# Performance work log

Hardware: AMD Instinct MI355X
Metric: run time of the kernel (lower is better)

Reference implementation:

```python
import jax, jax.numpy as jnp
import numpy as np

B, NS, S, H = 2048, 8, 8, 512   # batch, num_units, num_mem_slots, hidden==num_mem_size
WH, WK = 1, 32                  # write attention heads, key_size
RH, RK = 4, 32                  # read (mem) attention heads, mem_attention_key


def _lin(x, W, b):
    # torch nn.Linear convention: W is [out, in]
    return jnp.einsum('...i,oi->...o', x, W) + b


def setup_inputs() -> dict:
    key = jax.random.key(0)
    ks = jax.random.split(key, 13)
    def w(k, o, i):
        return jax.random.normal(k, (o, i), jnp.float32) * 0.02
    d = {
        'h_s': jax.random.normal(ks[0], (B, NS, H), jnp.float32),
        'mem': jax.random.normal(ks[1], (B, S, H), jnp.float32),
        'wq_w': w(ks[2], WH * WK, H), 'wq_b': jnp.zeros((WH * WK,), jnp.float32),
        'wk_w': w(ks[3], WH * WK, H), 'wk_b': jnp.zeros((WH * WK,), jnp.float32),
        'wv_w': w(ks[4], WH * H, H), 'wv_b': jnp.zeros((WH * H,), jnp.float32),
        'wo_w': w(ks[5], H, WH * H), 'wo_b': jnp.zeros((H,), jnp.float32),
        'ut_w': w(ks[6], H, H),      'ut_b': jnp.zeros((H,), jnp.float32),
        'ug_w': w(ks[7], 2 * H, H),  'ug_b': jnp.zeros((2 * H,), jnp.float32),
        'rq_w': w(ks[8], RH * RK, H), 'rq_b': jnp.zeros((RH * RK,), jnp.float32),
        'rk_w': w(ks[9], RH * RK, H), 'rk_b': jnp.zeros((RH * RK,), jnp.float32),
        'rv_w': w(ks[10], RH * H, H), 'rv_b': jnp.zeros((RH * H,), jnp.float32),
        'ro_w': w(ks[11], H, RH * H), 'ro_b': jnp.zeros((H,), jnp.float32),
    }
    return d


def _forward(h_s, mem, wq_w, wq_b, wk_w, wk_b, wv_w, wv_b, wo_w, wo_b,
             ut_w, ut_b, ug_w, ug_b, rq_w, rq_b, rk_w, rk_b, rv_w, rv_b,
             ro_w, ro_b):
    b = h_s.shape[0]
    T = NS + S  # concat length for write keys/values

    # ---------------- write ----------------
    xi = jnp.concatenate([h_s, mem], axis=1)                       # [B, T, H]
    q = _lin(mem, wq_w, wq_b).reshape(b, S, WH, WK).transpose(0, 2, 1, 3)   # [B,WH,S,WK]
    k = _lin(xi, wk_w, wk_b).reshape(b, T, WH, WK).transpose(0, 2, 1, 3)    # [B,WH,T,WK]
    v = _lin(xi, wv_w, wv_b).reshape(b, T, WH, H).transpose(0, 2, 1, 3)     # [B,WH,T,H]
    scores = jnp.einsum('bhsk,bhtk->bhst', q, k) / np.sqrt(WK).astype(np.float32)
    probs = jax.nn.softmax(scores, axis=-1)                         # [B,WH,S,T]
    ctx = jnp.einsum('bhst,bhtd->bhsd', probs, v)                   # [B,WH,S,H]
    ctx = ctx.transpose(0, 2, 1, 3).reshape(b, S, WH * H)
    mem_write = _lin(ctx, wo_w, wo_b)                               # [B,S,H]

    # ---------------- update (GRU-like gating) ----------------
    inputs_mean = jax.nn.relu(_lin(h_s, ut_w, ut_b)).mean(axis=1, keepdims=True)  # [B,1,H]
    kk = inputs_mean + jnp.tanh(mem)                                # [B,S,H]
    gates = jax.nn.sigmoid(_lin(kk, ug_w, ug_b))                    # [B,S,2H]
    input_gate, forget_gate = gates[..., :H], gates[..., H:]
    mem_new = input_gate * jnp.tanh(mem_write) + forget_gate * mem  # [B,S,H]

    # ---------------- read ----------------
    q = _lin(h_s, rq_w, rq_b).reshape(b, NS, RH, RK).transpose(0, 2, 1, 3)      # [B,RH,NS,RK]
    k = _lin(mem_new, rk_w, rk_b).reshape(b, S, RH, RK).transpose(0, 2, 1, 3)   # [B,RH,S,RK]
    v = _lin(mem_new, rv_w, rv_b).reshape(b, S, RH, H).transpose(0, 2, 1, 3)    # [B,RH,S,H]
    scores = jnp.einsum('bhnk,bhsk->bhns', q, k) / np.sqrt(RK).astype(np.float32)
    probs = jax.nn.softmax(scores, axis=-1)                          # [B,RH,NS,S]
    ctx = jnp.einsum('bhns,bhsd->bhnd', probs, v)                    # [B,RH,NS,H]
    ctx = ctx.transpose(0, 2, 1, 3).reshape(b, NS, RH * H)
    h_out = h_s + _lin(ctx, ro_w, ro_b)                              # residual
    return h_out, mem_new


def reference(h_s, mem, wq_w, wq_b, wk_w, wk_b, wv_w, wv_b, wo_w, wo_b,
              ut_w, ut_b, ug_w, ug_b, rq_w, rq_b, rk_w, rk_b, rv_w, rv_b,
              ro_w, ro_b):
    return _forward(h_s, mem, wq_w, wq_b, wk_w, wk_b, wv_w, wv_b, wo_w, wo_b,
                    ut_w, ut_b, ug_w, ug_b, rq_w, rq_b, rk_w, rk_b, rv_w, rv_b,
                    ro_w, ro_b)
```

## Files before the change

### kernel.cpp

```cpp
#include <hip/hip_runtime.h>

#define Bb   2048
#define Mrows 16384
#define Hd   512

typedef float  f32x4  __attribute__((ext_vector_type(4)));
typedef __bf16 bf16x8 __attribute__((ext_vector_type(8)));
typedef unsigned short us8 __attribute__((ext_vector_type(8)));

__device__ __forceinline__ unsigned short f2bf(float f) {
    unsigned int u = __builtin_bit_cast(unsigned int, f);
    u = u + 0x7FFFu + ((u >> 16) & 1u);
    return (unsigned short)(u >> 16);
}
__device__ __forceinline__ float bf2f(unsigned short h) {
    unsigned int u = ((unsigned int)h) << 16;
    return __builtin_bit_cast(float, u);
}

__device__ __forceinline__ void gload_lds16(const unsigned short* g, void* lds) {
    __builtin_amdgcn_global_load_lds(
        (const __attribute__((address_space(1))) unsigned int*)g,
        (__attribute__((address_space(3))) unsigned int*)lds,
        16, 0, 0);
}

#define MB (1024ull*1024ull)
#define OFF_WQ   0ull
#define OFF_WK   32768ull
#define OFF_WV   65536ull
#define OFF_WO   589824ull
#define OFF_UT   1114112ull
#define OFF_UG   1638400ull
#define OFF_RQ   2686976ull
#define OFF_RK   2818048ull
#define OFF_RV   2949120ull
#define OFF_RO   5046272ull
#define OFF_HS    (8*MB)
#define OFF_MEM   (24*MB)
#define OFF_UTR   (40*MB)
#define OFF_Q1    (60*MB)
#define OFF_K1    (62*MB)
#define OFF_V1    (66*MB)
#define OFF_CTX1  (100*MB)
#define OFF_KK    (116*MB)
#define OFF_TMW   (132*MB)
#define OFF_GATES (148*MB)
#define OFF_MNB   (180*MB)
#define OFF_Q2    (196*MB)
#define OFF_K2    (204*MB)
#define OFF_RVO   (40*MB)
#define OFF_CTX2  (104*MB)

struct CastSeg { const float* src; unsigned short* dst; int n4; };
struct CastParams { CastSeg seg[12]; };

__global__ __launch_bounds__(256) void cast_all(CastParams p) {
    CastSeg s = p.seg[blockIdx.y];
    int stride = gridDim.x * blockDim.x;
    for (int i = blockIdx.x * blockDim.x + threadIdx.x; i < s.n4; i += stride) {
        float4 v = reinterpret_cast<const float4*>(s.src)[i];
        ushort4 o;
        o.x = f2bf(v.x); o.y = f2bf(v.y); o.z = f2bf(v.z); o.w = f2bf(v.w);
        reinterpret_cast<ushort4*>(s.dst)[i] = o;
    }
}

template<int MODE>
__device__ __forceinline__ void store_c(void* out, const float* extra, int row,
                                        int col, int ldo, int remap_off, float v) {
    if (MODE == 0) {
        ((float*)out)[(size_t)row * ldo + col] = v;
    } else if (MODE == 1) {
        ((unsigned short*)out)[(size_t)row * ldo + col] = f2bf(v);
    } else if (MODE == 2) {
        ((unsigned short*)out)[(size_t)row * ldo + col] = f2bf(fmaxf(v, 0.f));
    } else if (MODE == 3) {
        ((unsigned short*)out)[(size_t)row * ldo + col] = f2bf(1.f / (1.f + expf(-v)));
    } else if (MODE == 4) {
        ((unsigned short*)out)[(size_t)row * ldo + col] = f2bf(tanhf(v));
    } else if (MODE == 5) {
        int rr = ((row >> 3) << 4) + (row & 7) + remap_off;
        ((float*)out)[(size_t)rr * ldo + col] = v;
    } else if (MODE == 6) {
        int rr = ((row >> 3) << 4) + (row & 7) + remap_off;
        ((unsigned short*)out)[(size_t)rr * ldo + col] = f2bf(v);
    } else if (MODE == 7) {
        ((float*)out)[(size_t)row * ldo + col] = v + extra[(size_t)row * ldo + col];
    }
}

struct GemmSeg {
    const unsigned short* A;
    const unsigned short* W;
    const float* bias;
    void* out;
    const float* extra;
    int mode, ldo, remap_off, tile0;
};
struct GemmParams { GemmSeg seg[4]; int nseg; int tiles_tot; };

template<int K>
__global__ __launch_bounds__(256, 4) void gemm_multi(GemmParams p)
{
    constexpr int NT = K / 32;
    __shared__ __align__(16) unsigned short As[2][128 * 32];
    __shared__ __align__(16) unsigned short Bs[2][128 * 32];

    const int nwg = (int)gridDim.x;
    const int swz = ((int)blockIdx.x & 7) * (nwg >> 3) + ((int)blockIdx.x >> 3);
    const int bm = swz / p.tiles_tot;
    const int tl = swz - bm * p.tiles_tot;

    int si = 0;
    #pragma unroll
    for (int i = 1; i < 4; i++)
        if (i < p.nseg && tl >= p.seg[i].tile0) si = i;
    const unsigned short* Aseg = p.seg[si].A;
    const unsigned short* Wseg = p.seg[si].W;
    const int bn = tl - p.seg[si].tile0;

    const int t = threadIdx.x;
    const int wave = t >> 6, lane = t & 63;
    const int wr = (wave >> 1) * 64;
    const int wc = (wave & 1) * 64;
    const int lrow = lane & 15;
    const int lkh  = lane >> 4;

    const unsigned short* ga[2];
    const unsigned short* gb[2];
    #pragma unroll
    for (int j = 0; j < 2; j++) {
        int c   = wave * 128 + j * 64 + lane;
        int row = c >> 2;
        int kl  = (c & 3) ^ (row & 3);
        ga[j] = Aseg + (size_t)(bm * 128 + row) * K + kl * 8;
        gb[j] = Wseg + (size_t)(bn * 128 + row) * K + kl * 8;
    }

    int aof[4], bof[4];
    #pragma unroll
    for (int m = 0; m < 4; m++) {
        int ra = wr + m * 16 + lrow;
        int rb = wc + m * 16 + lrow;
        aof[m] = ra * 32 + ((lkh ^ (ra & 3)) << 3);
        bof[m] = rb * 32 + ((lkh ^ (rb & 3)) << 3);
    }

    f32x4 acc[4][4] = {};

    #pragma unroll
    for (int j = 0; j < 2; j++) {
        gload_lds16(ga[j], (char*)As[0] + (wave * 2 + j) * 1024);
        gload_lds16(gb[j], (char*)Bs[0] + (wave * 2 + j) * 1024);
    }

    #pragma unroll 2
    for (int kt = 0; kt < NT; ++kt) {
        const int cur = kt & 1;
        asm volatile("s_waitcnt vmcnt(0)" ::: "memory");
        __builtin_amdgcn_s_barrier();
        __builtin_amdgcn_sched_barrier(0);
        if (kt + 1 < NT) {
            #pragma unroll
            for (int j = 0; j < 2; j++) {
                gload_lds16(ga[j] + (kt + 1) * 32, (char*)As[cur ^ 1] + (wave * 2 + j) * 1024);
                gload_lds16(gb[j] + (kt + 1) * 32, (char*)Bs[cur ^ 1] + (wave * 2 + j) * 1024);
            }
        }
        bf16x8 af[4], bfr[4];
        #pragma unroll
        for (int m = 0; m < 4; m++)
            af[m] = __builtin_bit_cast(bf16x8,
                        *reinterpret_cast<const us8*>(&As[cur][aof[m]]));
        #pragma unroll
        for (int n = 0; n < 4; n++)
            bfr[n] = __builtin_bit_cast(bf16x8,
                        *reinterpret_cast<const us8*>(&Bs[cur][bof[n]]));
        #pragma unroll
        for (int m = 0; m < 4; m++)
            #pragma unroll
            for (int n = 0; n < 4; n++)
                acc[m][n] = __builtin_amdgcn_mfma_f32_16x16x32_bf16(
                                af[m], bfr[n], acc[m][n], 0, 0, 0);
    }

    void* outp = p.seg[si].out;
    const float* bias = p.seg[si].bias;
    const float* extra = p.seg[si].extra;
    const int ldo = p.seg[si].ldo, rmo = p.seg[si].remap_off, mode = p.seg[si].mode;

    #define EPI(MODE_)                                                          \
        _Pragma("unroll")                                                       \
        for (int n = 0; n < 4; n++) {                                           \
            int col = bn * 128 + wc + n * 16 + lrow;                            \
            float bv = bias[col];                                               \
            _Pragma("unroll")                                                   \
            for (int m = 0; m < 4; m++) {                                       \
                _Pragma("unroll")                                               \
                for (int r = 0; r < 4; r++) {                                   \
                    int row = bm * 128 + wr + m * 16 + lkh * 4 + r;             \
                    store_c<MODE_>(outp, extra, row, col, ldo, rmo,             \
                                   acc[m][n][r] + bv);                          \
                }                                                               \
            }                                                                   \
        }
    switch (mode) {
        case 0: EPI(0) break;
        case 1: EPI(1) break;
        case 2: EPI(2) break;
        case 3: EPI(3) break;
        case 4: EPI(4) break;
        case 5: EPI(5) break;
        case 6: EPI(6) break;
        default: EPI(7) break;
    }
    #undef EPI
}

struct SmallSeg {
    const unsigned short* A;
    const unsigned short* W;
    const float* bias;
    float* out;
    int mode, remap_off;
};
struct SmallParams { SmallSeg seg[3]; };

__global__ __launch_bounds__(256) void gemm_small3(SmallParams p)
{
    constexpr int K = 512;
    const int si = blockIdx.x >> 8;
    const int bm = blockIdx.x & 255;
    const SmallSeg s = p.seg[si];

    const int wave = threadIdx.x >> 6;
    const int lane = threadIdx.x & 63;
    const int row0 = bm * 64 + wave * 16;
    const int lrow = lane & 15;
    const int lk   = (lane >> 4) << 3;

    f32x4 acc[2] = {};
    const unsigned short* ap  = s.A + (size_t)(row0 + lrow) * K + lk;
    const unsigned short* wp0 = s.W + (size_t)lrow * K + lk;

    #pragma unroll 4
    for (int ks = 0; ks < K; ks += 32) {
        bf16x8 af = __builtin_bit_cast(bf16x8,
                        *reinterpret_cast<const us8*>(ap + ks));
        #pragma unroll
        for (int tt = 0; tt < 2; tt++) {
            bf16x8 bfm = __builtin_bit_cast(bf16x8,
                        *reinterpret_cast<const us8*>(wp0 + (size_t)tt * 16 * K + ks));
            acc[tt] = __builtin_amdgcn_mfma_f32_16x16x32_bf16(af, bfm, acc[tt], 0, 0, 0);
        }
    }

    #pragma unroll
    for (int tt = 0; tt < 2; tt++) {
        int col = tt * 16 + lrow;
        float bv = s.bias[col];
        #pragma unroll
        for (int r = 0; r < 4; r++) {
            int row = row0 + (lane >> 4) * 4 + r;
            float v = acc[tt][r] + bv;
            if (s.mode == 0) {
                s.out[(size_t)row * 32 + col] = v;
            } else {
                int rr = ((row >> 3) << 4) + (row & 7) + s.remap_off;
                s.out[(size_t)rr * 32 + col] = v;
            }
        }
    }
}

__global__ __launch_bounds__(256) void meankk_kernel(
    const unsigned short* __restrict__ UTR, const float* __restrict__ mem,
    unsigned short* __restrict__ KK)
{
    int b = blockIdx.x;
    #pragma unroll
    for (int half = 0; half < 2; half++) {
        int j = threadIdx.x + half * 256;
        float sum = 0.f;
        #pragma unroll
        for (int r = 0; r < 8; r++)
            sum += bf2f(UTR[((size_t)(b * 8 + r) << 9) + j]);
        float mn = sum * 0.125f;
        #pragma unroll
        for (int r = 0; r < 8; r++) {
            size_t idx = ((size_t)(b * 8 + r) << 9) + j;
            KK[idx] = f2bf(mn + tanhf(mem[idx]));
        }
    }
}

__global__ __launch_bounds__(256) void memnew_kernel(
    const unsigned short* __restrict__ GATES, const unsigned short* __restrict__ TMW,
    const float* __restrict__ mem, float* __restrict__ out_mem,
    unsigned short* __restrict__ MNB)
{
    int idx = blockIdx.x * 256 + threadIdx.x;
    int m = idx >> 7, j4 = idx & 127;
    ushort4 ig4 = reinterpret_cast<const ushort4*>(GATES + (size_t)m * 1024)[j4];
    ushort4 fg4 = reinterpret_cast<const ushort4*>(GATES + (size_t)m * 1024 + 512)[j4];
    ushort4 tm4 = reinterpret_cast<const ushort4*>(TMW + (size_t)m * 512)[j4];
    float4  mm  = reinterpret_cast<const float4*>(mem + (size_t)m * 512)[j4];
    float4 v;
    v.x = bf2f(ig4.x) * bf2f(tm4.x) + bf2f(fg4.x) * mm.x;
    v.y = bf2f(ig4.y) * bf2f(tm4.y) + bf2f(fg4.y) * mm.y;
    v.z = bf2f(ig4.z) * bf2f(tm4.z) + bf2f(fg4.z) * mm.z;
    v.w = bf2f(ig4.w) * bf2f(tm4.w) + bf2f(fg4.w) * mm.w;
    reinterpret_cast<float4*>(out_mem + (size_t)m * 512)[j4] = v;
    ushort4 o; o.x = f2bf(v.x); o.y = f2bf(v.y); o.z = f2bf(v.z); o.w = f2bf(v.w);
    reinterpret_cast<ushort4*>(MNB + (size_t)m * 512)[j4] = o;
}

__global__ __launch_bounds__(256) void attn1_kernel(
    const float* __restrict__ Q1, const float* __restrict__ K1,
    const unsigned short* __restrict__ V1, unsigned short* __restrict__ CTX1)
{
    int b = blockIdx.x, t = threadIdx.x;
    __shared__ float q[8][32], k[16][32], pr[8][16];
    q[t >> 5][t & 31] = Q1[(size_t)b * 256 + t];
    k[t >> 5][t & 31]       = K1[(size_t)b * 512 + t];
    k[8 + (t >> 5)][t & 31] = K1[(size_t)b * 512 + 256 + t];
    __syncthreads();
    if (t < 128) {
        int s = t >> 4, tt = t & 15;
        float acc = 0.f;
        #pragma unroll
        for (int i = 0; i < 32; i++) acc += q[s][i] * k[tt][i];
        pr[s][tt] = acc * 0.17677669529663687f;
    }
    __syncthreads();
    if (t < 8) {
        float m = -1e30f;
        for (int i = 0; i < 16; i++) m = fmaxf(m, pr[t][i]);
        float e[16], sum = 0.f;
        for (int i = 0; i < 16; i++) { e[i] = expf(pr[t][i] - m); sum += e[i]; }
        float inv = 1.f / sum;
        for (int i = 0; i < 16; i++) pr[t][i] = e[i] * inv;
    }
    __syncthreads();
    int s = t >> 5, d0 = (t & 31) * 16;
    float a[16];
    #pragma unroll
    for (int i = 0; i < 16; i++) a[i] = 0.f;
    for (int tt = 0; tt < 16; tt++) {
        float p = pr[s][tt];
        const unsigned short* vp = V1 + ((size_t)(b * 16 + tt)) * 512 + d0;
        us8 v0 = *reinterpret_cast<const us8*>(vp);
        us8 v1 = *reinterpret_cast<const us8*>(vp + 8);
        #pragma unroll
        for (int i = 0; i < 8; i++) a[i]     += p * bf2f(v0[i]);
        #pragma unroll
        for (int i = 0; i < 8; i++) a[8 + i] += p * bf2f(v1[i]);
    }
    us8 o0, o1;
    #pragma unroll
    for (int i = 0; i < 8; i++) { o0[i] = f2bf(a[i]); o1[i] = f2bf(a[8 + i]); }
    unsigned short* cp = CTX1 + ((size_t)(b * 8 + s)) * 512 + d0;
    *reinterpret_cast<us8*>(cp) = o0;
    *reinterpret_cast<us8*>(cp + 8) = o1;
}

__global__ __launch_bounds__(256) void attn2_kernel(
    const float* __restrict__ Q2, const float* __restrict__ K2,
    const unsigned short* __restrict__ V2, unsigned short* __restrict__ CTX2)
{
    int b = blockIdx.x, t = threadIdx.x;
    __shared__ float q[8][128], k[8][128], pr[4][8][8];
    for (int i = t; i < 1024; i += 256) {
        q[i >> 7][i & 127] = Q2[(size_t)b * 1024 + i];
        k[i >> 7][i & 127] = K2[(size_t)b * 1024 + i];
    }
    __syncthreads();
    {
        int h = t >> 6, n = (t >> 3) & 7, s = t & 7;
        float acc = 0.f;
        #pragma unroll
        for (int i = 0; i < 32; i++) acc += q[n][h * 32 + i] * k[s][h * 32 + i];
        pr[h][n][s] = acc * 0.17677669529663687f;
    }
    __syncthreads();
    if (t < 32) {
        int h = t >> 3, n = t & 7;
        float m = -1e30f;
        for (int i = 0; i < 8; i++) m = fmaxf(m, pr[h][n][i]);
        float e[8], sum = 0.f;
        for (int i = 0; i < 8; i++) { e[i] = expf(pr[h][n][i] - m); sum += e[i]; }
        float inv = 1.f / sum;
        for (int i = 0; i < 8; i++) pr[h][n][i] = e[i] * inv;
    }
    __syncthreads();
    int n = t >> 5, d0 = (t & 31) * 16;
    for (int h = 0; h < 4; h++) {
        float a[16];
        #pragma unroll
        for (int i = 0; i < 16; i++) a[i] = 0.f;
        for (int s = 0; s < 8; s++) {
            float p = pr[h][n][s];
            const unsigned short* vp = V2 + ((size_t)(b * 8 + s)) * 2048 + h * 512 + d0;
            us8 v0 = *reinterpret_cast<const us8*>(vp);
            us8 v1 = *reinterpret_cast<const us8*>(vp + 8);
            #pragma unroll
            for (int i = 0; i < 8; i++) a[i]     += p * bf2f(v0[i]);
            #pragma unroll
            for (int i = 0; i < 8; i++) a[8 + i] += p * bf2f(v1[i]);
        }
        us8 o0, o1;
        #pragma unroll
        for (int i = 0; i < 8; i++) { o0[i] = f2bf(a[i]); o1[i] = f2bf(a[8 + i]); }
        unsigned short* cp = CTX2 + ((size_t)(b * 8 + n)) * 2048 + h * 512 + d0;
        *reinterpret_cast<us8*>(cp) = o0;
        *reinterpret_cast<us8*>(cp + 8) = o1;
    }
}

extern "C" void kernel_launch(void* const* d_in, const int* in_sizes, int n_in,
                              void* d_out, int out_size, void* d_ws, size_t ws_size,
                              hipStream_t stream)
{
    const float* h_s  = (const float*)d_in[0];
    const float* mem  = (const float*)d_in[1];
    const float* wq_w = (const float*)d_in[2];  const float* wq_b = (const float*)d_in[3];
    const float* wk_w = (const float*)d_in[4];  const float* wk_b = (const float*)d_in[5];
    const float* wv_w = (const float*)d_in[6];  const float* wv_b = (const float*)d_in[7];
    const float* wo_w = (const float*)d_in[8];  const float* wo_b = (const float*)d_in[9];
    const float* ut_w = (const float*)d_in[10]; const float* ut_b = (const float*)d_in[11];
    const float* ug_w = (const float*)d_in[12]; const float* ug_b = (const float*)d_in[13];
    const float* rq_w = (const float*)d_in[14]; const float* rq_b = (const float*)d_in[15];
    const float* rk_w = (const float*)d_in[16]; const float* rk_b = (const float*)d_in[17];
    const float* rv_w = (const float*)d_in[18]; const float* rv_b = (const float*)d_in[19];
    const float* ro_w = (const float*)d_in[20]; const float* ro_b = (const float*)d_in[21];

    char* ws = (char*)d_ws;
    unsigned short* WQb = (unsigned short*)(ws + OFF_WQ);
    unsigned short* WKb = (unsigned short*)(ws + OFF_WK);
    unsigned short* WVb = (unsigned short*)(ws + OFF_WV);
    unsigned short* WOb = (unsigned short*)(ws + OFF_WO);
    unsigned short* UTb = (unsigned short*)(ws + OFF_UT);
    unsigned short* UGb = (unsigned short*)(ws + OFF_UG);
    unsigned short* RQb = (unsigned short*)(ws + OFF_RQ);
    unsigned short* RKb = (unsigned short*)(ws + OFF_RK);
    unsigned short* RVb = (unsigned short*)(ws + OFF_RV);
    unsigned short* ROb = (unsigned short*)(ws + OFF_RO);
    unsigned short* HSb  = (unsigned short*)(ws + OFF_HS);
    unsigned short* MEMb = (unsigned short*)(ws + OFF_MEM);
    unsigned short* UTR  = (unsigned short*)(ws + OFF_UTR);
    float*          Q1   = (float*)(ws + OFF_Q1);
    float*          K1   = (float*)(ws + OFF_K1);
    unsigned short* V1   = (unsigned short*)(ws + OFF_V1);
    unsigned short* CTX1 = (unsigned short*)(ws + OFF_CTX1);
    unsigned short* KKb  = (unsigned short*)(ws + OFF_KK);
    unsigned short* TMW  = (unsigned short*)(ws + OFF_TMW);
    unsigned short* GATES= (unsigned short*)(ws + OFF_GATES);
    unsigned short* MNB  = (unsigned short*)(ws + OFF_MNB);
    float*          Q2   = (float*)(ws + OFF_Q2);
    float*          K2   = (float*)(ws + OFF_K2);
    unsigned short* RVO  = (unsigned short*)(ws + OFF_RVO);
    unsigned short* CTX2 = (unsigned short*)(ws + OFF_CTX2);

    float* out   = (float*)d_out;
    float* out_m = out + (size_t)Mrows * Hd;

    CastParams cp;
    cp.seg[0]  = { h_s,  HSb,  (Mrows * Hd) / 4 };
    cp.seg[1]  = { mem,  MEMb, (Mrows * Hd) / 4 };
    cp.seg[2]  = { wq_w, WQb,  (32 * 512) / 4 };
    cp.seg[3]  = { wk_w, WKb,  (32 * 512) / 4 };
    cp.seg[4]  = { wv_w, WVb,  (512 * 512) / 4 };
    cp.seg[5]  = { wo_w, WOb,  (512 * 512) / 4 };
    cp.seg[6]  = { ut_w, UTb,  (512 * 512) / 4 };
    cp.seg[7]  = { ug_w, UGb,  (1024 * 512) / 4 };
    cp.seg[8]  = { rq_w, RQb,  (128 * 512) / 4 };
    cp.seg[9]  = { rk_w, RKb,  (128 * 512) / 4 };
    cp.seg[10] = { rv_w, RVb,  (2048 * 512) / 4 };
    cp.seg[11] = { ro_w, ROb,  (512 * 2048) / 4 };
    cast_all<<<dim3(2048, 12), 256, 0, stream>>>(cp);

    {
        GemmParams g;
        g.seg[0] = { HSb,  UTb, ut_b, UTR, nullptr, 2, 512,  0, 0 };
        g.seg[1] = { HSb,  WVb, wv_b, V1,  nullptr, 6, 512,  0, 4 };
        g.seg[2] = { HSb,  RQb, rq_b, Q2,  nullptr, 0, 128,  0, 8 };
        g.seg[3] = { MEMb, WVb, wv_b, V1,  nullptr, 6, 512,  8, 9 };
        g.nseg = 4; g.tiles_tot = 13;
        gemm_multi<512><<<128 * 13, 256, 0, stream>>>(g);
    }
    {
        SmallParams sp;
        sp.seg[0] = { HSb,  WKb, wk_b, K1, 5, 0 };
        sp.seg[1] = { MEMb, WQb, wq_b, Q1, 0, 0 };
        sp.seg[2] = { MEMb, WKb, wk_b, K1, 5, 8 };
        gemm_small3<<<768, 256, 0, stream>>>(sp);
    }

    meankk_kernel<<<Bb, 256, 0, stream>>>(UTR, mem, KKb);

    attn1_kernel<<<Bb, 256, 0, stream>>>(Q1, K1, V1, CTX1);

    {
        GemmParams g;
        g.seg[0] = { CTX1, WOb, wo_b, TMW,   nullptr, 4,  512, 0, 0 };
        g.seg[1] = { KKb,  UGb, ug_b, GATES, nullptr, 3, 1024, 0, 4 };
        g.nseg = 2; g.tiles_tot = 12;
        gemm_multi<512><<<128 * 12, 256, 0, stream>>>(g);
    }

    memnew_kernel<<<8192, 256, 0, stream>>>(GATES, TMW, mem, out_m, MNB);

    {
        GemmParams g;
        g.seg[0] = { MNB, RKb, rk_b, K2,  nullptr, 0,  128, 0, 0 };
        g.seg[1] = { MNB, RVb, rv_b, RVO, nullptr, 1, 2048, 0, 1 };
        g.nseg = 2; g.tiles_tot = 17;
        gemm_multi<512><<<128 * 17, 256, 0, stream>>>(g);
    }

    attn2_kernel<<<Bb, 256, 0, stream>>>(Q2, K2, RVO, CTX2);

    {
        GemmParams g;
        g.seg[0] = { CTX2, ROb, ro_b, out, h_s, 7, 512, 0, 0 };
        g.nseg = 1; g.tiles_tot = 4;
        gemm_multi<2048><<<128 * 4, 256, 0, stream>>>(g);
    }

    (void)in_sizes; (void)n_in; (void)out_size; (void)ws_size;
}
```

Measured before the change: 524.5 us.

## Switch GEMM to single-buffered 64-wide K tiles with higher occupancy

Replaces the double-buffered 32-wide K staging with a single LDS buffer holding 64-wide K tiles, using 8-way XOR swizzle and two MFMA sub-steps per iteration. Launch bounds are raised to target 5 workgroups per CU, so occupancy rather than in-block prefetch hides load latency. This halves the loop iterations and barrier count, but the global-to-LDS loads no longer overlap compute inside a workgroup, and register pressure may rise.

```diff
diff --git a/kernel.cpp b/kernel.cpp
--- a/kernel.cpp
+++ b/kernel.cpp
@@ -101,11 +101,11 @@
 struct GemmParams { GemmSeg seg[4]; int nseg; int tiles_tot; };
 
 template<int K>
-__global__ __launch_bounds__(256, 4) void gemm_multi(GemmParams p)
-{
-    constexpr int NT = K / 32;
-    __shared__ __align__(16) unsigned short As[2][128 * 32];
-    __shared__ __align__(16) unsigned short Bs[2][128 * 32];
+__global__ __launch_bounds__(256, 5) void gemm_multi(GemmParams p)
+{
+    constexpr int NT = K / 64;
+    __shared__ __align__(16) unsigned short As[128 * 64];
+    __shared__ __align__(16) unsigned short Bs[128 * 64];
 
     const int nwg = (int)gridDim.x;
     const int swz = ((int)blockIdx.x & 7) * (nwg >> 3) + ((int)blockIdx.x >> 3);
@@ -127,62 +127,66 @@
     const int lrow = lane & 15;
     const int lkh  = lane >> 4;
 
-    const unsigned short* ga[2];
-    const unsigned short* gb[2];
-    #pragma unroll
-    for (int j = 0; j < 2; j++) {
-        int c   = wave * 128 + j * 64 + lane;
-        int row = c >> 2;
-        int kl  = (c & 3) ^ (row & 3);
+    const unsigned short* ga[4];
+    const unsigned short* gb[4];
+    #pragma unroll
+    for (int j = 0; j < 4; j++) {
+        int c   = wave * 256 + j * 64 + lane;
+        int row = c >> 3;
+        int kl  = (c & 7) ^ (row & 7);
         ga[j] = Aseg + (size_t)(bm * 128 + row) * K + kl * 8;
         gb[j] = Wseg + (size_t)(bn * 128 + row) * K + kl * 8;
     }
 
-    int aof[4], bof[4];
+    int aof[4][2], bof[4][2];
     #pragma unroll
     for (int m = 0; m < 4; m++) {
         int ra = wr + m * 16 + lrow;
         int rb = wc + m * 16 + lrow;
-        aof[m] = ra * 32 + ((lkh ^ (ra & 3)) << 3);
-        bof[m] = rb * 32 + ((lkh ^ (rb & 3)) << 3);
+        #pragma unroll
+        for (int kk = 0; kk < 2; kk++) {
+            int kc = kk * 4 + lkh;
+            aof[m][kk] = ra * 64 + ((kc ^ (ra & 7)) << 3);
+            bof[m][kk] = rb * 64 + ((kc ^ (rb & 7)) << 3);
+        }
     }
 
     f32x4 acc[4][4] = {};
 
     #pragma unroll
-    for (int j = 0; j < 2; j++) {
-        gload_lds16(ga[j], (char*)As[0] + (wave * 2 + j) * 1024);
-        gload_lds16(gb[j], (char*)Bs[0] + (wave * 2 + j) * 1024);
-    }
-
-    #pragma unroll 2
+    for (int j = 0; j < 4; j++) {
+        gload_lds16(ga[j], (char*)As + (wave * 4 + j) * 1024);
+        gload_lds16(gb[j], (char*)Bs + (wave * 4 + j) * 1024);
+    }
+
     for (int kt = 0; kt < NT; ++kt) {
-        const int cur = kt & 1;
-        asm volatile("s_waitcnt vmcnt(0)" ::: "memory");
-        __builtin_amdgcn_s_barrier();
-        __builtin_amdgcn_sched_barrier(0);
+        __syncthreads();
+        #pragma unroll
+        for (int kk = 0; kk < 2; kk++) {
+            bf16x8 af[4], bfr[4];
+            #pragma unroll
+            for (int m = 0; m < 4; m++)
+                af[m] = __builtin_bit_cast(bf16x8,
+                            *reinterpret_cast<const us8*>(&As[aof[m][kk]]));
+            #pragma unroll
+            for (int n = 0; n < 4; n++)
+                bfr[n] = __builtin_bit_cast(bf16x8,
+                            *reinterpret_cast<const us8*>(&Bs[bof[n][kk]]));
+            #pragma unroll
+            for (int m = 0; m < 4; m++)
+                #pragma unroll
+                for (int n = 0; n < 4; n++)
+                    acc[m][n] = __builtin_amdgcn_mfma_f32_16x16x32_bf16(
+                                    af[m], bfr[n], acc[m][n], 0, 0, 0);
+        }
+        __syncthreads();
         if (kt + 1 < NT) {
             #pragma unroll
-            for (int j = 0; j < 2; j++) {
-                gload_lds16(ga[j] + (kt + 1) * 32, (char*)As[cur ^ 1] + (wave * 2 + j) * 1024);
-                gload_lds16(gb[j] + (kt + 1) * 32, (char*)Bs[cur ^ 1] + (wave * 2 + j) * 1024);
+            for (int j = 0; j < 4; j++) {
+                gload_lds16(ga[j] + (kt + 1) * 64, (char*)As + (wave * 4 + j) * 1024);
+                gload_lds16(gb[j] + (kt + 1) * 64, (char*)Bs + (wave * 4 + j) * 1024);
             }
         }
-        bf16x8 af[4], bfr[4];
-        #pragma unroll
-        for (int m = 0; m < 4; m++)
-            af[m] = __builtin_bit_cast(bf16x8,
-                        *reinterpret_cast<const us8*>(&As[cur][aof[m]]));
-        #pragma unroll
-        for (int n = 0; n < 4; n++)
-            bfr[n] = __builtin_bit_cast(bf16x8,
-                        *reinterpret_cast<const us8*>(&Bs[cur][bof[n]]));
-        #pragma unroll
-        for (int m = 0; m < 4; m++)
-            #pragma unroll
-            for (int n = 0; n < 4; n++)
-                acc[m][n] = __builtin_amdgcn_mfma_f32_16x16x32_bf16(
-                                af[m], bfr[n], acc[m][n], 0, 0, 0);
     }
 
     void* outp = p.seg[si].out;
```

Result: slower. 726.5 us (+38.5%).
